# Optimization experiments

Measured on AMD Instinct MI355X. Metric: run time of the kernel, lower is better.

Reference implementation:

```python
import jax, jax.numpy as jnp
import numpy as np
import math

EMBED_DIM = 512
NUM_HEADS = 8
B, T = 1, 4096

def setup_inputs() -> dict:
    key = jax.random.key(0)
    ks = jax.random.split(key, 12)
    D = EMBED_DIM
    s = 1.0 / math.sqrt(D)
    inp = {
        "x": jax.random.normal(ks[0], (B, T, D), dtype=jnp.float32),
        "ln1_scale": jnp.ones((D,), jnp.float32),
        "ln1_bias": jnp.zeros((D,), jnp.float32),
        "Wq": jax.random.normal(ks[1], (D, D), jnp.float32) * s,
        "bq": jnp.zeros((D,), jnp.float32),
        "Wk": jax.random.normal(ks[2], (D, D), jnp.float32) * s,
        "bk": jnp.zeros((D,), jnp.float32),
        "Wv": jax.random.normal(ks[3], (D, D), jnp.float32) * s,
        "bv": jnp.zeros((D,), jnp.float32),
        "Wo": jax.random.normal(ks[4], (D, D), jnp.float32) * s,
        "bo": jnp.zeros((D,), jnp.float32),
        "ln2_scale": jnp.ones((D,), jnp.float32),
        "ln2_bias": jnp.zeros((D,), jnp.float32),
        "W1": jax.random.normal(ks[5], (D, 4 * D), jnp.float32) * s,
        "b1": jnp.zeros((4 * D,), jnp.float32),
        "W2": jax.random.normal(ks[6], (4 * D, D), jnp.float32) * (1.0 / math.sqrt(4 * D)),
        "b2": jnp.zeros((D,), jnp.float32),
    }
    return inp

def _layernorm(x, scale, bias, eps=1e-6):
    mu = jnp.mean(x, axis=-1, keepdims=True)
    var = jnp.mean(jnp.square(x - mu), axis=-1, keepdims=True)
    return (x - mu) * jax.lax.rsqrt(var + eps) * scale + bias

def reference(x, ln1_scale, ln1_bias, Wq, bq, Wk, bk, Wv, bv, Wo, bo,
              ln2_scale, ln2_bias, W1, b1, W2, b2):
    Bb, Tt, D = x.shape
    H = NUM_HEADS
    hd = D // H
    residual = x
    h = _layernorm(x, ln1_scale, ln1_bias)
    q = (h @ Wq + bq).reshape(Bb, Tt, H, hd).transpose(0, 2, 1, 3)
    k = (h @ Wk + bk).reshape(Bb, Tt, H, hd).transpose(0, 2, 1, 3)
    v = (h @ Wv + bv).reshape(Bb, Tt, H, hd).transpose(0, 2, 1, 3)
    # [B,H,T,T] scores (naive attention as in the original module)
    scores = jnp.einsum('bhqd,bhkd->bhqk', q, k) / math.sqrt(hd)
    probs = jax.nn.softmax(scores, axis=-1)
    out = jnp.einsum('bhqk,bhkd->bhqd', probs, v).transpose(0, 2, 1, 3).reshape(Bb, Tt, D)
    h = out @ Wo + bo  # dropout deterministic -> identity
    x = h + residual
    residual = x
    h = _layernorm(x, ln2_scale, ln2_bias)
    h = jax.nn.gelu(h @ W1 + b1, approximate=True)
    h = h @ W2 + b2
    return h + residual
```

## Files before the change

kernel.cpp:

```cpp
#include <hip/hip_runtime.h>
#include <hip/hip_bf16.h>
#include <stdint.h>

typedef __bf16 bf16;
typedef __bf16 bf16x4 __attribute__((ext_vector_type(4)));
typedef __bf16 bf16x8 __attribute__((ext_vector_type(8)));
typedef float  f32x4  __attribute__((ext_vector_type(4)));
typedef float  f32x16 __attribute__((ext_vector_type(16)));

#define MFMA16(A_, B_, C_) __builtin_amdgcn_mfma_f32_16x16x32_bf16((A_), (B_), (C_), 0, 0, 0)
#define MFMA32(A_, B_, C_) __builtin_amdgcn_mfma_f32_32x32x16_bf16((A_), (B_), (C_), 0, 0, 0)

#define QSCALE 0.1803368801111137f

__device__ __forceinline__ void gload_lds16(const void* g, void* l) {
  __builtin_amdgcn_global_load_lds(
      (const __attribute__((address_space(1))) unsigned int*)g,
      (__attribute__((address_space(3))) unsigned int*)l, 16, 0, 0);
}

__device__ __forceinline__ unsigned pk2(float lo, float hi_) {
  union { bf16 h[2]; unsigned u; } t;
  t.h[0] = (bf16)lo; t.h[1] = (bf16)hi_;
  return t.u;
}

__device__ __forceinline__ float fast_exp2(float x) {
#if __has_builtin(__builtin_amdgcn_exp2f)
  return __builtin_amdgcn_exp2f(x);
#else
  return exp2f(x);
#endif
}

__global__ __launch_bounds__(256) void prep(const float* __restrict__ Wq,
                                            const float* __restrict__ Wk,
                                            const float* __restrict__ Wv,
                                            const float* __restrict__ Wo,
                                            const float* __restrict__ W1,
                                            const float* __restrict__ W2,
                                            const float* __restrict__ bq,
                                            const float* __restrict__ bk,
                                            const float* __restrict__ bv,
                                            bf16* __restrict__ wqkvT, bf16* __restrict__ woT,
                                            bf16* __restrict__ w1T, bf16* __restrict__ w2T,
                                            float* __restrict__ bqkv) {
  const int b = blockIdx.x;
  if (b >= 768) {
    int i = (b - 768) * 256 + threadIdx.x;
    if (i < 1536)
      bqkv[i] = (i < 512) ? bq[i] * QSCALE : (i < 1024 ? bk[i - 512] : bv[i - 1024]);
    return;
  }
  const float* in; bf16* outp; int K, N, t; float sc = 1.f;
  if (b < 64)       { in = Wq; outp = wqkvT;              K = 512;  N = 512;  t = b;       sc = QSCALE; }
  else if (b < 128) { in = Wk; outp = wqkvT + 512 * 512;  K = 512;  N = 512;  t = b - 64;  }
  else if (b < 192) { in = Wv; outp = wqkvT + 1024 * 512; K = 512;  N = 512;  t = b - 128; }
  else if (b < 256) { in = Wo; outp = woT;                K = 512;  N = 512;  t = b - 192; }
  else if (b < 512) { in = W1; outp = w1T;                K = 512;  N = 2048; t = b - 256; }
  else              { in = W2; outp = w2T;                K = 2048; N = 512;  t = b - 512; }
  const int tx = K >> 6;
  const int k0 = (t % tx) * 64, n0 = (t / tx) * 64;
  __shared__ bf16 tile[64][72];
  const int tid = threadIdx.x;
#pragma unroll
  for (int s = 0; s < 16; ++s) {
    int j = tid + s * 256;
    int r = j >> 6, c = j & 63;
    tile[r][c] = (bf16)(in[(size_t)(k0 + r) * N + n0 + c] * sc);
  }
  __syncthreads();
#pragma unroll
  for (int s = 0; s < 16; ++s) {
    int j = tid + s * 256;
    int n = j >> 6, k = j & 63;
    outp[(size_t)(n0 + n) * K + k0 + k] = tile[k][n];
  }
}

__global__ __launch_bounds__(256) void ln_k(const float* __restrict__ x,
                                            const float* __restrict__ sc,
                                            const float* __restrict__ bi,
                                            bf16* __restrict__ out) {
  const int w = threadIdx.x >> 6, l = threadIdx.x & 63;
  const int row = blockIdx.x * 4 + w;
  const float4* xp = (const float4*)(x + (size_t)row * 512 + l * 8);
  float4 v0 = xp[0], v1 = xp[1];
  float xv[8] = {v0.x, v0.y, v0.z, v0.w, v1.x, v1.y, v1.z, v1.w};
  float s = 0.f, q = 0.f;
#pragma unroll
  for (int j = 0; j < 8; ++j) { s += xv[j]; q += xv[j] * xv[j]; }
#pragma unroll
  for (int m = 1; m < 64; m <<= 1) { s += __shfl_xor(s, m); q += __shfl_xor(q, m); }
  const float mean = s * (1.f / 512.f);
  const float var = q * (1.f / 512.f) - mean * mean;
  const float rstd = rsqrtf(var + 1e-6f);
  const float4* scp = (const float4*)(sc + l * 8);
  const float4* bip = (const float4*)(bi + l * 8);
  float4 s0 = scp[0], s1 = scp[1], b0 = bip[0], b1 = bip[1];
  float sv[8] = {s0.x, s0.y, s0.z, s0.w, s1.x, s1.y, s1.z, s1.w};
  float bv[8] = {b0.x, b0.y, b0.z, b0.w, b1.x, b1.y, b1.z, b1.w};
  bf16x8 ov;
#pragma unroll
  for (int j = 0; j < 8; ++j) ov[j] = (bf16)((xv[j] - mean) * rstd * sv[j] + bv[j]);
  *(bf16x8*)(out + (size_t)row * 512 + l * 8) = ov;
}

__global__ __launch_bounds__(256) void ln2_comb(const float* __restrict__ p0,
                                                const float* __restrict__ p1,
                                                const float* __restrict__ x,
                                                const float* __restrict__ bo,
                                                const float* __restrict__ sc,
                                                const float* __restrict__ bi,
                                                float* __restrict__ x2,
                                                bf16* __restrict__ h2) {
  const int w = threadIdx.x >> 6, l = threadIdx.x & 63;
  const int row = blockIdx.x * 4 + w;
  const size_t base = (size_t)row * 512 + l * 8;
  float xv[8];
#pragma unroll
  for (int j = 0; j < 2; ++j) {
    float4 a = *(const float4*)(p0 + base + j * 4);
    float4 b = *(const float4*)(p1 + base + j * 4);
    float4 c = *(const float4*)(x + base + j * 4);
    float4 d = *(const float4*)(bo + l * 8 + j * 4);
    xv[j * 4 + 0] = a.x + b.x + c.x + d.x;
    xv[j * 4 + 1] = a.y + b.y + c.y + d.y;
    xv[j * 4 + 2] = a.z + b.z + c.z + d.z;
    xv[j * 4 + 3] = a.w + b.w + c.w + d.w;
  }
  *(float4*)(x2 + base) = make_float4(xv[0], xv[1], xv[2], xv[3]);
  *(float4*)(x2 + base + 4) = make_float4(xv[4], xv[5], xv[6], xv[7]);
  float s = 0.f, q = 0.f;
#pragma unroll
  for (int j = 0; j < 8; ++j) { s += xv[j]; q += xv[j] * xv[j]; }
#pragma unroll
  for (int m = 1; m < 64; m <<= 1) { s += __shfl_xor(s, m); q += __shfl_xor(q, m); }
  const float mean = s * (1.f / 512.f);
  const float var = q * (1.f / 512.f) - mean * mean;
  const float rstd = rsqrtf(var + 1e-6f);
  const float4* scp = (const float4*)(sc + l * 8);
  const float4* bip = (const float4*)(bi + l * 8);
  float4 s0 = scp[0], s1 = scp[1], b0 = bip[0], b1 = bip[1];
  float sv[8] = {s0.x, s0.y, s0.z, s0.w, s1.x, s1.y, s1.z, s1.w};
  float bv[8] = {b0.x, b0.y, b0.z, b0.w, b1.x, b1.y, b1.z, b1.w};
  bf16x8 ov;
#pragma unroll
  for (int j = 0; j < 8; ++j) ov[j] = (bf16)((xv[j] - mean) * rstd * sv[j] + bv[j]);
  *(bf16x8*)(h2 + base) = ov;
}

__global__ __launch_bounds__(256) void final_comb(const float* __restrict__ parts, int nsplit,
                                                  const float* __restrict__ b2,
                                                  const float* __restrict__ x2,
                                                  float* __restrict__ outp) {
  const int i4 = blockIdx.x * 256 + threadIdx.x;
  const size_t off = (size_t)i4 * 4;
  float4 acc = *(const float4*)(x2 + off);
  float4 bb = *(const float4*)(b2 + (off & 511));
  acc.x += bb.x; acc.y += bb.y; acc.z += bb.z; acc.w += bb.w;
  for (int z = 0; z < nsplit; ++z) {
    float4 p = *(const float4*)(parts + (size_t)z * 4096 * 512 + off);
    acc.x += p.x; acc.y += p.y; acc.z += p.z; acc.w += p.w;
  }
  *(float4*)(outp + off) = acc;
}

template <int EPI>
__global__ __launch_bounds__(256) void gemm_bt(const bf16* __restrict__ A,
                                               const bf16* __restrict__ Bt,
                                               const float* __restrict__ bias,
                                               const float* __restrict__ res,
                                               void* __restrict__ outp,
                                               int M, int N, int K) {
  __shared__ bf16 a_lds[128 * 64];
  __shared__ bf16 b_lds[128 * 64];
  const int m0 = blockIdx.x * 128, n0 = blockIdx.y * 128;
  const int tid = threadIdx.x, l = tid & 63, w = tid >> 6;
  const int wm = w >> 1, wn = w & 1;
  const int lc = l & 15, g = l >> 4;
  const int srow = l >> 3;
  const int cs = (l & 7) ^ srow;

  f32x4 acc[4][4] = {};
  const int kiters = K >> 6;
  for (int kt = 0; kt < kiters; ++kt) {
    const int k0 = kt << 6;
#pragma unroll
    for (int r = 0; r < 4; ++r) {
      const int rg = r * 32 + w * 8;
      gload_lds16(A + (size_t)(m0 + rg + srow) * K + k0 + cs * 8,
                  (char*)a_lds + rg * 128);
      gload_lds16(Bt + (size_t)(n0 + rg + srow) * K + k0 + cs * 8,
                  (char*)b_lds + rg * 128);
    }
    __syncthreads();
#pragma unroll
    for (int kk = 0; kk < 2; ++kk) {
      bf16x8 af[4], bfr[4];
#pragma unroll
      for (int i = 0; i < 4; ++i) {
        const int sw = ((kk * 4 + g) ^ (lc & 7)) * 8;
        af[i]  = *(const bf16x8*)(a_lds + (wm * 64 + i * 16 + lc) * 64 + sw);
        bfr[i] = *(const bf16x8*)(b_lds + (wn * 64 + i * 16 + lc) * 64 + sw);
      }
#pragma unroll
      for (int mi = 0; mi < 4; ++mi)
#pragma unroll
        for (int ni = 0; ni < 4; ++ni)
          acc[mi][ni] = MFMA16(af[mi], bfr[ni], acc[mi][ni]);
    }
    __syncthreads();
  }

#pragma unroll
  for (int mi = 0; mi < 4; ++mi)
#pragma unroll
    for (int ni = 0; ni < 4; ++ni) {
      const int col = n0 + wn * 64 + ni * 16 + lc;
      const float bb = bias[col];
#pragma unroll
      for (int i = 0; i < 4; ++i) {
        const int row = m0 + wm * 64 + mi * 16 + g * 4 + i;
        float v = acc[mi][ni][i] + bb;
        if constexpr (EPI == 0) {
          ((bf16*)outp)[(size_t)row * N + col] = (bf16)v;
        } else if constexpr (EPI == 1) {
          ((float*)outp)[(size_t)row * N + col] = v + res[(size_t)row * N + col];
        } else {
          float t = -2.3022077697f * (v + 0.044715f * v * v * v);
          float gl = v / (1.f + fast_exp2(t));
          ((bf16*)outp)[(size_t)row * N + col] = (bf16)gl;
        }
      }
    }
}

__global__ __launch_bounds__(256) void gemm_skp(const bf16* __restrict__ A,
                                                const bf16* __restrict__ Bt,
                                                float* __restrict__ parts,
                                                int M, int N, int Kstride, int Kc) {
  __shared__ bf16 a_lds[128 * 64];
  __shared__ bf16 b_lds[128 * 64];
  const int m0 = blockIdx.x * 128, n0 = blockIdx.y * 128, kz = blockIdx.z;
  A += (size_t)kz * Kc;
  Bt += (size_t)kz * Kc;
  float* outp = parts + (size_t)kz * M * N;
  const int tid = threadIdx.x, l = tid & 63, w = tid >> 6;
  const int wm = w >> 1, wn = w & 1;
  const int lc = l & 15, g = l >> 4;
  const int srow = l >> 3;
  const int cs = (l & 7) ^ srow;

  f32x4 acc[4][4] = {};
  const int kiters = Kc >> 6;
  for (int kt = 0; kt < kiters; ++kt) {
    const int k0 = kt << 6;
#pragma unroll
    for (int r = 0; r < 4; ++r) {
      const int rg = r * 32 + w * 8;
      gload_lds16(A + (size_t)(m0 + rg + srow) * Kstride + k0 + cs * 8,
                  (char*)a_lds + rg * 128);
      gload_lds16(Bt + (size_t)(n0 + rg + srow) * Kstride + k0 + cs * 8,
                  (char*)b_lds + rg * 128);
    }
    __syncthreads();
#pragma unroll
    for (int kk = 0; kk < 2; ++kk) {
      bf16x8 af[4], bfr[4];
#pragma unroll
      for (int i = 0; i < 4; ++i) {
        const int sw = ((kk * 4 + g) ^ (lc & 7)) * 8;
        af[i]  = *(const bf16x8*)(a_lds + (wm * 64 + i * 16 + lc) * 64 + sw);
        bfr[i] = *(const bf16x8*)(b_lds + (wn * 64 + i * 16 + lc) * 64 + sw);
      }
#pragma unroll
      for (int mi = 0; mi < 4; ++mi)
#pragma unroll
        for (int ni = 0; ni < 4; ++ni)
          acc[mi][ni] = MFMA16(af[mi], bfr[ni], acc[mi][ni]);
    }
    __syncthreads();
  }

#pragma unroll
  for (int mi = 0; mi < 4; ++mi)
#pragma unroll
    for (int ni = 0; ni < 4; ++ni) {
      const int col = n0 + wn * 64 + ni * 16 + lc;
#pragma unroll
      for (int i = 0; i < 4; ++i) {
        const int row = m0 + wm * 64 + mi * 16 + g * 4 + i;
        outp[(size_t)row * N + col] = acc[mi][ni][i];
      }
    }
}

__global__ __launch_bounds__(256) void repack(const bf16* __restrict__ qkv,
                                              bf16* __restrict__ k2,
                                              bf16* __restrict__ v2) {
  __shared__ bf16 tile[64][72];
  const int t0 = blockIdx.x * 64;
  const int head = blockIdx.y;
  const int tid = threadIdx.x;
#pragma unroll
  for (int s = 0; s < 16; ++s) {
    int j = tid + s * 256;
    int t = j >> 6, d = j & 63;
    k2[(size_t)head * 262144 + (size_t)(t0 + t) * 64 + d] =
        qkv[(size_t)(t0 + t) * 1536 + 512 + head * 64 + d];
  }
#pragma unroll
  for (int s = 0; s < 16; ++s) {
    int j = tid + s * 256;
    int t = j >> 6, c = j & 63;
    tile[t][c] = qkv[(size_t)(t0 + t) * 1536 + 1024 + head * 64 + c];
  }
  __syncthreads();
#pragma unroll
  for (int s = 0; s < 16; ++s) {
    int j = tid + s * 256;
    int d = j >> 6, t = j & 63;
    v2[(size_t)head * 262144 + (size_t)((t0 >> 5) + (t >> 5)) * 2048 + d * 32 + (t & 31)] =
        tile[t][d];
  }
}

__global__ __launch_bounds__(256, 4) void attn_k(const bf16* __restrict__ qkv,
                                                 const bf16* __restrict__ k2,
                                                 const bf16* __restrict__ v2,
                                                 bf16* __restrict__ opart,
                                                 float* __restrict__ lpart) {
  const int bid = blockIdx.x;
  const int head = bid & 7;
  const int qt = (bid >> 3) & 63;
  const int ks = bid >> 9;
  const int w = threadIdx.x >> 6, l = threadIdx.x & 63;
  const int hi = l >> 5, l5 = l & 31;
  const int pair = w >> 1, wq = w & 1;

  __shared__ __align__(16) char smem[32768];
  char* kt_l = smem + pair * 16384;
  char* vt_l = kt_l + 8192;

  const int qrow0 = qt * 64 + wq * 32;
  const bf16* qb = qkv + (size_t)(qrow0 + l5) * 1536 + head * 64;
  bf16x8 qf[4];
#pragma unroll
  for (int cc = 0; cc < 4; ++cc) qf[cc] = *(const bf16x8*)(qb + cc * 16 + hi * 8);

  const int kstart = ks * 2048 + pair * 1024;

  const int lr = l >> 3;
  const int lc3 = (l & 7) ^ lr;
  const char* kg = (const char*)k2 + (size_t)head * 524288 + (size_t)kstart * 128 +
                   (wq * 16 + lr) * 128 + lc3 * 16;
  const char* vg = (const char*)v2 + (size_t)head * 524288 + (size_t)(kstart >> 5) * 4096 +
                   (lc3 >> 2) * 2048 + (wq * 16 + lr) * 64 + (lc3 & 3) * 16;
  const int kdst = wq * 2048;

#define STAGE(B_)                                                            \
  do {                                                                       \
    gload_lds16(kg,        kt_l + (B_) * 4096 + kdst);                       \
    gload_lds16(kg + 1024, kt_l + (B_) * 4096 + kdst + 1024);                \
    gload_lds16(vg,        vt_l + (B_) * 4096 + kdst);                       \
    gload_lds16(vg + 512,  vt_l + (B_) * 4096 + kdst + 1024);                \
    kg += 4096; vg += 4096;                                                  \
  } while (0)

  STAGE(0);
  __syncthreads();

  f32x16 o0 = {}, o1 = {};
  float psum = 0.f;
  const int swl = l5 & 7;
  const char* kbase = kt_l + l5 * 128;
  const char* vbase = vt_l + l5 * 128;

  for (int t = 0; t < 32; ++t) {
    const int cur = t & 1;
    if (t < 31) STAGE(cur ^ 1);

    __builtin_amdgcn_s_setprio(1);
    f32x16 s = {};
#pragma unroll
    for (int cc = 0; cc < 4; ++cc) {
      bf16x8 kf = *(const bf16x8*)(kbase + cur * 4096 + ((cc * 2 + hi) ^ swl) * 16);
      s = MFMA32(kf, qf[cc], s);
    }
    __builtin_amdgcn_s_setprio(0);

#pragma unroll
    for (int c = 0; c < 2; ++c) {
      float p[8];
#pragma unroll
      for (int j = 0; j < 8; ++j) p[j] = fast_exp2(s[c * 8 + j]);
      psum += ((p[0] + p[1]) + (p[2] + p[3])) + ((p[4] + p[5]) + (p[6] + p[7]));
      unsigned X = pk2(p[0], p[1]), X2 = pk2(p[2], p[3]);
      unsigned Y = pk2(p[4], p[5]), Y2 = pk2(p[6], p[7]);
      asm volatile("v_permlane32_swap_b32 %0, %1" : "+v"(X), "+v"(Y));
      asm volatile("v_permlane32_swap_b32 %0, %1" : "+v"(X2), "+v"(Y2));
      union { unsigned wd[4]; bf16x8 v; } pa;
      pa.wd[0] = X; pa.wd[1] = X2; pa.wd[2] = Y; pa.wd[3] = Y2;
      bf16x8 vf0 = *(const bf16x8*)(vbase + cur * 4096 + ((c * 2 + hi) ^ swl) * 16);
      bf16x8 vf1 = *(const bf16x8*)(vbase + cur * 4096 + ((4 + c * 2 + hi) ^ swl) * 16);
      __builtin_amdgcn_s_setprio(1);
      o0 = MFMA32(vf0, pa.v, o0);
      o1 = MFMA32(vf1, pa.v, o1);
      __builtin_amdgcn_s_setprio(0);
    }
    __syncthreads();
  }
#undef STAGE

  float* comb = (float*)smem;
  if (w >= 2) {
    float* cb = comb + ((w - 2) * 64 + l) * 33;
#pragma unroll
    for (int r = 0; r < 16; ++r) { cb[r] = o0[r]; cb[16 + r] = o1[r]; }
    cb[32] = psum;
  }
  __syncthreads();
  if (w < 2) {
    const float* cb = comb + (w * 64 + l) * 33;
#pragma unroll
    for (int r = 0; r < 16; ++r) { o0[r] += cb[r]; o1[r] += cb[16 + r]; }
    psum += cb[32];
    const float lsum = psum + __shfl_xor(psum, 32);
    bf16* ob = opart + (size_t)ks * 4096 * 512 + (size_t)(qrow0 + l5) * 512 + head * 64;
#pragma unroll
    for (int dt = 0; dt < 2; ++dt)
#pragma unroll
      for (int rg = 0; rg < 4; ++rg) {
        bf16x4 vv;
#pragma unroll
        for (int e = 0; e < 4; ++e) {
          const float ov = (dt == 0) ? o0[rg * 4 + e] : o1[rg * 4 + e];
          vv[e] = (bf16)ov;
        }
        *(bf16x4*)(ob + dt * 32 + rg * 8 + hi * 4) = vv;
      }
    if (hi == 0) lpart[(ks * 8 + head) * 4096 + qrow0 + l5] = lsum;
  }
}

__global__ __launch_bounds__(256) void attn_comb(const bf16* __restrict__ op,
                                                 const float* __restrict__ lp,
                                                 bf16* __restrict__ ob) {
  const int idx = blockIdx.x * 256 + threadIdx.x;
  const int t = idx >> 6, c8 = idx & 63;
  const int head = c8 >> 3;
  const size_t o = (size_t)t * 512 + c8 * 8;
  bf16x8 a = *(const bf16x8*)(op + o);
  bf16x8 b = *(const bf16x8*)(op + 2097152 + o);
  const float inv = 1.f / (lp[head * 4096 + t] + lp[32768 + head * 4096 + t]);
  bf16x8 r;
#pragma unroll
  for (int j = 0; j < 8; ++j) r[j] = (bf16)(((float)a[j] + (float)b[j]) * inv);
  *(bf16x8*)(ob + o) = r;
}

extern "C" void kernel_launch(void* const* d_in, const int* in_sizes, int n_in,
                              void* d_out, int out_size, void* d_ws, size_t ws_size,
                              hipStream_t stream) {
  const float* x    = (const float*)d_in[0];
  const float* ln1s = (const float*)d_in[1];
  const float* ln1b = (const float*)d_in[2];
  const float* Wq   = (const float*)d_in[3];
  const float* bq   = (const float*)d_in[4];
  const float* Wk   = (const float*)d_in[5];
  const float* bk   = (const float*)d_in[6];
  const float* Wv   = (const float*)d_in[7];
  const float* bv   = (const float*)d_in[8];
  const float* Wo   = (const float*)d_in[9];
  const float* bo   = (const float*)d_in[10];
  const float* ln2s = (const float*)d_in[11];
  const float* ln2b = (const float*)d_in[12];
  const float* W1   = (const float*)d_in[13];
  const float* b1   = (const float*)d_in[14];
  const float* W2   = (const float*)d_in[15];
  const float* b2   = (const float*)d_in[16];
  float* out = (float*)d_out;

  char* ws = (char*)d_ws;
  bf16*  wqkvT = (bf16*)(ws + 0);
  bf16*  woT   = (bf16*)(ws + 1572864);
  bf16*  w1T   = (bf16*)(ws + 2097152);
  bf16*  w2T   = (bf16*)(ws + 4194304);
  float* bqkv  = (float*)(ws + 6291456);
  float* lpart = (float*)(ws + 6297600);
  bf16*  opart = (bf16*)(ws + 6559744);
  float* x2    = (float*)(ws + 6559744);
  bf16*  h     = (bf16*)(ws + 14948352);
  bf16*  qkv   = (bf16*)(ws + 19142656);
  bf16*  k2    = (bf16*)(ws + 31725568);
  bf16*  v2    = (bf16*)(ws + 35919872);
  bf16*  attnb = h;
  bf16*  h2    = h;
  float* wop   = (float*)(ws + 19142656);
  bf16*  gbuf  = qkv;
  float* f2p   = (float*)(ws + 40114176);
  const size_t need4 = 40114176 + 4ull * 8388608;
  const size_t need2 = 40114176 + 2ull * 8388608;

  prep<<<774, 256, 0, stream>>>(Wq, Wk, Wv, Wo, W1, W2, bq, bk, bv,
                                wqkvT, woT, w1T, w2T, bqkv);

  ln_k<<<1024, 256, 0, stream>>>(x, ln1s, ln1b, h);
  gemm_bt<0><<<dim3(32, 12), 256, 0, stream>>>(h, wqkvT, bqkv, nullptr, qkv, 4096, 1536, 512);
  repack<<<dim3(64, 8), 256, 0, stream>>>(qkv, k2, v2);
  attn_k<<<1024, 256, 0, stream>>>(qkv, k2, v2, opart, lpart);
  attn_comb<<<1024, 256, 0, stream>>>(opart, lpart, attnb);
  gemm_skp<<<dim3(32, 4, 2), 256, 0, stream>>>(attnb, woT, wop, 4096, 512, 512, 256);
  ln2_comb<<<1024, 256, 0, stream>>>(wop, wop + 4096 * 512, x, bo, ln2s, ln2b, x2, h2);
  gemm_bt<2><<<dim3(32, 16), 256, 0, stream>>>(h2, w1T, b1, nullptr, gbuf, 4096, 2048, 512);
  if (ws_size >= need4) {
    gemm_skp<<<dim3(32, 4, 4), 256, 0, stream>>>(gbuf, w2T, f2p, 4096, 512, 2048, 512);
    final_comb<<<2048, 256, 0, stream>>>(f2p, 4, b2, x2, out);
  } else if (ws_size >= need2) {
    gemm_skp<<<dim3(32, 4, 2), 256, 0, stream>>>(gbuf, w2T, f2p, 4096, 512, 2048, 1024);
    final_comb<<<2048, 256, 0, stream>>>(f2p, 2, b2, x2, out);
  } else {
    gemm_bt<1><<<dim3(32, 4), 256, 0, stream>>>(gbuf, w2T, b2, x2, out, 4096, 512, 2048);
  }
}
```

Before: 148.7 us.

## Double-buffer GEMM LDS staging and fuse K/V repack into QKV GEMM epilogue

Both GEMM kernels now use two LDS buffers, so the global-to-LDS load for the next K tile is issued while MFMAs run on the current tile, and one barrier per iteration is removed. The QKV projection epilogue now writes Q to a compact buffer and scatters K and V directly into the per-head layouts attention expects, which removes the separate repack kernel and its extra pass over memory. The workspace layout is shrunk to match. Costs are doubled LDS per block (64 KB), which may lower occupancy, and scattered narrow bf16 stores for the V transpose layout.

```diff
diff --git a/kernel.cpp b/kernel.cpp
--- a/kernel.cpp
+++ b/kernel.cpp
@@ -172,9 +172,11 @@
                                                const float* __restrict__ bias,
                                                const float* __restrict__ res,
                                                void* __restrict__ outp,
+                                               bf16* __restrict__ k2,
+                                               bf16* __restrict__ v2,
                                                int M, int N, int K) {
-  __shared__ bf16 a_lds[128 * 64];
-  __shared__ bf16 b_lds[128 * 64];
+  __shared__ bf16 a_lds[2][128 * 64];
+  __shared__ bf16 b_lds[2][128 * 64];
   const int m0 = blockIdx.x * 128, n0 = blockIdx.y * 128;
   const int tid = threadIdx.x, l = tid & 63, w = tid >> 6;
   const int wm = w >> 1, wn = w & 1;
@@ -182,27 +184,37 @@
   const int srow = l >> 3;
   const int cs = (l & 7) ^ srow;
 
+  const bf16* ag = A + (size_t)(m0 + w * 8 + srow) * K + cs * 8;
+  const bf16* bg = Bt + (size_t)(n0 + w * 8 + srow) * K + cs * 8;
+  const size_t rstep = (size_t)32 * K;
+
+#define GSTAGE(B_)                                                       \
+  do {                                                                   \
+    _Pragma("unroll")                                                    \
+    for (int r_ = 0; r_ < 4; ++r_) {                                     \
+      gload_lds16(ag + r_ * rstep, (char*)a_lds[B_] + (r_ * 32 + w * 8) * 128); \
+      gload_lds16(bg + r_ * rstep, (char*)b_lds[B_] + (r_ * 32 + w * 8) * 128); \
+    }                                                                    \
+    ag += 64; bg += 64;                                                  \
+  } while (0)
+
   f32x4 acc[4][4] = {};
   const int kiters = K >> 6;
+  GSTAGE(0);
+  __syncthreads();
   for (int kt = 0; kt < kiters; ++kt) {
-    const int k0 = kt << 6;
-#pragma unroll
-    for (int r = 0; r < 4; ++r) {
-      const int rg = r * 32 + w * 8;
-      gload_lds16(A + (size_t)(m0 + rg + srow) * K + k0 + cs * 8,
-                  (char*)a_lds + rg * 128);
-      gload_lds16(Bt + (size_t)(n0 + rg + srow) * K + k0 + cs * 8,
-                  (char*)b_lds + rg * 128);
-    }
-    __syncthreads();
+    const int cur = kt & 1;
+    if (kt + 1 < kiters) GSTAGE(cur ^ 1);
+    const bf16* ab = a_lds[cur];
+    const bf16* bb2 = b_lds[cur];
 #pragma unroll
     for (int kk = 0; kk < 2; ++kk) {
       bf16x8 af[4], bfr[4];
 #pragma unroll
       for (int i = 0; i < 4; ++i) {
         const int sw = ((kk * 4 + g) ^ (lc & 7)) * 8;
-        af[i]  = *(const bf16x8*)(a_lds + (wm * 64 + i * 16 + lc) * 64 + sw);
-        bfr[i] = *(const bf16x8*)(b_lds + (wn * 64 + i * 16 + lc) * 64 + sw);
+        af[i]  = *(const bf16x8*)(ab + (wm * 64 + i * 16 + lc) * 64 + sw);
+        bfr[i] = *(const bf16x8*)(bb2 + (wn * 64 + i * 16 + lc) * 64 + sw);
       }
 #pragma unroll
       for (int mi = 0; mi < 4; ++mi)
@@ -212,6 +224,7 @@
     }
     __syncthreads();
   }
+#undef GSTAGE
 
 #pragma unroll
   for (int mi = 0; mi < 4; ++mi)
@@ -223,14 +236,23 @@
       for (int i = 0; i < 4; ++i) {
         const int row = m0 + wm * 64 + mi * 16 + g * 4 + i;
         float v = acc[mi][ni][i] + bb;
-        if constexpr (EPI == 0) {
-          ((bf16*)outp)[(size_t)row * N + col] = (bf16)v;
-        } else if constexpr (EPI == 1) {
+        if constexpr (EPI == 1) {
           ((float*)outp)[(size_t)row * N + col] = v + res[(size_t)row * N + col];
-        } else {
+        } else if constexpr (EPI == 2) {
           float t = -2.3022077697f * (v + 0.044715f * v * v * v);
           float gl = v / (1.f + fast_exp2(t));
           ((bf16*)outp)[(size_t)row * N + col] = (bf16)gl;
+        } else {
+          const bf16 bv16 = (bf16)v;
+          if (col < 512) {
+            ((bf16*)outp)[(size_t)row * 512 + col] = bv16;
+          } else if (col < 1024) {
+            const int hd = (col - 512) >> 6, d = col & 63;
+            k2[(size_t)hd * 262144 + (size_t)row * 64 + d] = bv16;
+          } else {
+            const int hd = (col - 1024) >> 6, d = col & 63;
+            v2[(size_t)hd * 262144 + (size_t)(row >> 5) * 2048 + d * 32 + (row & 31)] = bv16;
+          }
         }
       }
     }
@@ -240,8 +262,8 @@
                                                 const bf16* __restrict__ Bt,
                                                 float* __restrict__ parts,
                                                 int M, int N, int Kstride, int Kc) {
-  __shared__ bf16 a_lds[128 * 64];
-  __shared__ bf16 b_lds[128 * 64];
+  __shared__ bf16 a_lds[2][128 * 64];
+  __shared__ bf16 b_lds[2][128 * 64];
   const int m0 = blockIdx.x * 128, n0 = blockIdx.y * 128, kz = blockIdx.z;
   A += (size_t)kz * Kc;
   Bt += (size_t)kz * Kc;
@@ -252,27 +274,37 @@
   const int srow = l >> 3;
   const int cs = (l & 7) ^ srow;
 
+  const bf16* ag = A + (size_t)(m0 + w * 8 + srow) * Kstride + cs * 8;
+  const bf16* bg = Bt + (size_t)(n0 + w * 8 + srow) * Kstride + cs * 8;
+  const size_t rstep = (size_t)32 * Kstride;
+
+#define GSTAGE(B_)                                                       \
+  do {                                                                   \
+    _Pragma("unroll")                                                    \
+    for (int r_ = 0; r_ < 4; ++r_) {                                     \
+      gload_lds16(ag + r_ * rstep, (char*)a_lds[B_] + (r_ * 32 + w * 8) * 128); \
+      gload_lds16(bg + r_ * rstep, (char*)b_lds[B_] + (r_ * 32 + w * 8) * 128); \
+    }                                                                    \
+    ag += 64; bg += 64;                                                  \
+  } while (0)
+
   f32x4 acc[4][4] = {};
   const int kiters = Kc >> 6;
+  GSTAGE(0);
+  __syncthreads();
   for (int kt = 0; kt < kiters; ++kt) {
-    const int k0 = kt << 6;
-#pragma unroll
-    for (int r = 0; r < 4; ++r) {
-      const int rg = r * 32 + w * 8;
-      gload_lds16(A + (size_t)(m0 + rg + srow) * Kstride + k0 + cs * 8,
-                  (char*)a_lds + rg * 128);
-      gload_lds16(Bt + (size_t)(n0 + rg + srow) * Kstride + k0 + cs * 8,
-                  (char*)b_lds + rg * 128);
-    }
-    __syncthreads();
+    const int cur = kt & 1;
+    if (kt + 1 < kiters) GSTAGE(cur ^ 1);
+    const bf16* ab = a_lds[cur];
+    const bf16* bb2 = b_lds[cur];
 #pragma unroll
     for (int kk = 0; kk < 2; ++kk) {
       bf16x8 af[4], bfr[4];
 #pragma unroll
       for (int i = 0; i < 4; ++i) {
         const int sw = ((kk * 4 + g) ^ (lc & 7)) * 8;
-        af[i]  = *(const bf16x8*)(a_lds + (wm * 64 + i * 16 + lc) * 64 + sw);
-        bfr[i] = *(const bf16x8*)(b_lds + (wn * 64 + i * 16 + lc) * 64 + sw);
+        af[i]  = *(const bf16x8*)(ab + (wm * 64 + i * 16 + lc) * 64 + sw);
+        bfr[i] = *(const bf16x8*)(bb2 + (wn * 64 + i * 16 + lc) * 64 + sw);
       }
 #pragma unroll
       for (int mi = 0; mi < 4; ++mi)
@@ -282,6 +314,7 @@
     }
     __syncthreads();
   }
+#undef GSTAGE
 
 #pragma unroll
   for (int mi = 0; mi < 4; ++mi)
@@ -296,37 +329,7 @@
     }
 }
 
-__global__ __launch_bounds__(256) void repack(const bf16* __restrict__ qkv,
-                                              bf16* __restrict__ k2,
-                                              bf16* __restrict__ v2) {
-  __shared__ bf16 tile[64][72];
-  const int t0 = blockIdx.x * 64;
-  const int head = blockIdx.y;
-  const int tid = threadIdx.x;
-#pragma unroll
-  for (int s = 0; s < 16; ++s) {
-    int j = tid + s * 256;
-    int t = j >> 6, d = j & 63;
-    k2[(size_t)head * 262144 + (size_t)(t0 + t) * 64 + d] =
-        qkv[(size_t)(t0 + t) * 1536 + 512 + head * 64 + d];
-  }
-#pragma unroll
-  for (int s = 0; s < 16; ++s) {
-    int j = tid + s * 256;
-    int t = j >> 6, c = j & 63;
-    tile[t][c] = qkv[(size_t)(t0 + t) * 1536 + 1024 + head * 64 + c];
-  }
-  __syncthreads();
-#pragma unroll
-  for (int s = 0; s < 16; ++s) {
-    int j = tid + s * 256;
-    int d = j >> 6, t = j & 63;
-    v2[(size_t)head * 262144 + (size_t)((t0 >> 5) + (t >> 5)) * 2048 + d * 32 + (t & 31)] =
-        tile[t][d];
-  }
-}
-
-__global__ __launch_bounds__(256, 4) void attn_k(const bf16* __restrict__ qkv,
+__global__ __launch_bounds__(256, 4) void attn_k(const bf16* __restrict__ q2,
                                                  const bf16* __restrict__ k2,
                                                  const bf16* __restrict__ v2,
                                                  bf16* __restrict__ opart,
@@ -344,7 +347,7 @@
   char* vt_l = kt_l + 8192;
 
   const int qrow0 = qt * 64 + wq * 32;
-  const bf16* qb = qkv + (size_t)(qrow0 + l5) * 1536 + head * 64;
+  const bf16* qb = q2 + (size_t)(qrow0 + l5) * 512 + head * 64;
   bf16x8 qf[4];
 #pragma unroll
   for (int cc = 0; cc < 4; ++cc) qf[cc] = *(const bf16x8*)(qb + cc * 16 + hi * 8);
@@ -488,32 +491,33 @@
   bf16*  w1T   = (bf16*)(ws + 2097152);
   bf16*  w2T   = (bf16*)(ws + 4194304);
   float* bqkv  = (float*)(ws + 6291456);
-  float* lpart = (float*)(ws + 6297600);
-  bf16*  opart = (bf16*)(ws + 6559744);
-  float* x2    = (float*)(ws + 6559744);
-  bf16*  h     = (bf16*)(ws + 14948352);
-  bf16*  qkv   = (bf16*)(ws + 19142656);
-  bf16*  k2    = (bf16*)(ws + 31725568);
-  bf16*  v2    = (bf16*)(ws + 35919872);
+  float* lpart = (float*)(ws + 6299648);
+  bf16*  opart = (bf16*)(ws + 6561792);
+  float* x2    = (float*)(ws + 6561792);
+  bf16*  h     = (bf16*)(ws + 14950400);
+  bf16*  q2    = (bf16*)(ws + 19144704);
+  bf16*  k2    = (bf16*)(ws + 23339008);
+  bf16*  v2    = (bf16*)(ws + 27533312);
   bf16*  attnb = h;
   bf16*  h2    = h;
-  float* wop   = (float*)(ws + 19142656);
-  bf16*  gbuf  = qkv;
-  float* f2p   = (float*)(ws + 40114176);
-  const size_t need4 = 40114176 + 4ull * 8388608;
-  const size_t need2 = 40114176 + 2ull * 8388608;
+  float* wop   = (float*)(ws + 19144704);
+  bf16*  gbuf  = (bf16*)(ws + 19144704);
+  float* f2p   = (float*)(ws + 35921920);
+  const size_t need4 = 35921920 + 4ull * 8388608;
+  const size_t need2 = 35921920 + 2ull * 8388608;
 
   prep<<<774, 256, 0, stream>>>(Wq, Wk, Wv, Wo, W1, W2, bq, bk, bv,
                                 wqkvT, woT, w1T, w2T, bqkv);
 
   ln_k<<<1024, 256, 0, stream>>>(x, ln1s, ln1b, h);
-  gemm_bt<0><<<dim3(32, 12), 256, 0, stream>>>(h, wqkvT, bqkv, nullptr, qkv, 4096, 1536, 512);
-  repack<<<dim3(64, 8), 256, 0, stream>>>(qkv, k2, v2);
-  attn_k<<<1024, 256, 0, stream>>>(qkv, k2, v2, opart, lpart);
+  gemm_bt<3><<<dim3(32, 12), 256, 0, stream>>>(h, wqkvT, bqkv, nullptr, q2, k2, v2,
+                                               4096, 1536, 512);
+  attn_k<<<1024, 256, 0, stream>>>(q2, k2, v2, opart, lpart);
   attn_comb<<<1024, 256, 0, stream>>>(opart, lpart, attnb);
   gemm_skp<<<dim3(32, 4, 2), 256, 0, stream>>>(attnb, woT, wop, 4096, 512, 512, 256);
   ln2_comb<<<1024, 256, 0, stream>>>(wop, wop + 4096 * 512, x, bo, ln2s, ln2b, x2, h2);
-  gemm_bt<2><<<dim3(32, 16), 256, 0, stream>>>(h2, w1T, b1, nullptr, gbuf, 4096, 2048, 512);
+  gemm_bt<2><<<dim3(32, 16), 256, 0, stream>>>(h2, w1T, b1, nullptr, gbuf, nullptr, nullptr,
+                                               4096, 2048, 512);
   if (ws_size >= need4) {
     gemm_skp<<<dim3(32, 4, 4), 256, 0, stream>>>(gbuf, w2T, f2p, 4096, 512, 2048, 512);
     final_comb<<<2048, 256, 0, stream>>>(f2p, 4, b2, x2, out);
@@ -521,6 +525,7 @@
     gemm_skp<<<dim3(32, 4, 2), 256, 0, stream>>>(gbuf, w2T, f2p, 4096, 512, 2048, 1024);
     final_comb<<<2048, 256, 0, stream>>>(f2p, 2, b2, x2, out);
   } else {
-    gemm_bt<1><<<dim3(32, 4), 256, 0, stream>>>(gbuf, w2T, b2, x2, out, 4096, 512, 2048);
-  }
-}
+    gemm_bt<1><<<dim3(32, 4), 256, 0, stream>>>(gbuf, w2T, b2, x2, out, nullptr, nullptr,
+                                                4096, 512, 2048);
+  }
+}
```

Result: no change. 147.7 us (-0.7%).
